# Performance work log

Hardware: AMD Instinct MI355X
Metric: run time of the kernel (lower is better)

Reference implementation:

```python
import jax, jax.numpy as jnp
import numpy as np
import math

B, S, D = 1, 2048, 2048
H, HD, KV = 16, 128, 1
E, F, TOPK = 8, 4096, 2
EPS = 1e-5


def setup_inputs() -> dict:
    key = jax.random.key(0)
    ks = jax.random.split(key, 14)
    sc = 0.02
    inp = {
        "x": jax.random.normal(ks[0], (B, S, D), dtype=jnp.float32),
        "wq": jax.random.normal(ks[1], (D, H * HD), dtype=jnp.float32) * sc,
        "wk": jax.random.normal(ks[2], (D, KV * HD), dtype=jnp.float32) * sc,
        "wv": jax.random.normal(ks[3], (D, KV * HD), dtype=jnp.float32) * sc,
        "wo": jax.random.normal(ks[4], (H * HD, D), dtype=jnp.float32) * sc,
        "w_router": jax.random.normal(ks[5], (D, E), dtype=jnp.float32) * sc,
        "w1": jax.random.normal(ks[6], (E, D, F), dtype=jnp.float32) * sc,
        "w3": jax.random.normal(ks[7], (E, D, F), dtype=jnp.float32) * sc,
        "w2": jax.random.normal(ks[8], (E, F, D), dtype=jnp.float32) * sc,
        "s_pre_mqa": jnp.ones((D,), dtype=jnp.float32),
        "s_post_mqa": jnp.ones((D,), dtype=jnp.float32),
        "s_pre_moe": jnp.ones((D,), dtype=jnp.float32),
        "s_post_moe": jnp.ones((D,), dtype=jnp.float32),
    }
    return inp


def _rmsnorm(x, scale):
    ms = jnp.mean(x * x, axis=-1, keepdims=True)
    return x * jax.lax.rsqrt(ms + EPS) * scale


def _mqa(h, wq, wk, wv, wo):
    b, s, _ = h.shape
    q = (h @ wq).reshape(b, s, H, HD)
    k = (h @ wk).reshape(b, s, KV, HD)
    v = (h @ wv).reshape(b, s, KV, HD)
    # repeat_interleave kv heads up to H (MQA)
    k = jnp.repeat(k, H // KV, axis=2)
    v = jnp.repeat(v, H // KV, axis=2)
    scale = 1.0 / math.sqrt(HD)
    scores = jnp.einsum("bqhd,bkhd->bhqk", q, k) * scale  # [B,H,S,S]
    causal = jnp.tril(jnp.ones((s, s), dtype=bool))
    scores = jnp.where(causal, scores, jnp.float32(-jnp.inf))
    attn = jax.nn.softmax(scores, axis=-1)
    out = jnp.einsum("bhqk,bkhd->bqhd", attn, v).reshape(b, s, H * HD)
    return out @ wo


def _moe(h, w_router, w1, w2, w3):
    logits = h @ w_router                        # [B,S,E]
    probs = jax.nn.softmax(logits, axis=-1)
    topv, topi = jax.lax.top_k(probs, TOPK)      # [B,S,K]
    topv = topv / jnp.sum(topv, axis=-1, keepdims=True)
    # combine weights per expert: [B,S,E]
    combine = jnp.sum(jax.nn.one_hot(topi, E, dtype=h.dtype) * topv[..., None], axis=-2)
    out = jnp.zeros_like(h)
    for e in range(E):  # fixed small expert count
        ye = (jax.nn.silu(h @ w1[e]) * (h @ w3[e])) @ w2[e]
        out = out + combine[..., e:e + 1] * ye
    return out, combine


def reference(x, wq, wk, wv, wo, w_router, w1, w2, w3,
              s_pre_mqa, s_post_mqa, s_pre_moe, s_post_moe):
    mqa_out = _mqa(_rmsnorm(x, s_pre_mqa), wq, wk, wv, wo)
    x = x + _rmsnorm(mqa_out, s_post_mqa)  # dropout p=0 (eval)
    moe_out, router_mask = _moe(_rmsnorm(x, s_pre_moe), w_router, w1, w2, w3)
    x = x + _rmsnorm(moe_out, s_post_moe)
    return x, router_mask
```

## Files before the change

### kernel.cpp

```cpp
#include <hip/hip_runtime.h>

#define S_LEN 2048
#define DM 2048
#define NHEAD 16
#define HDIM 128
#define NEXP 8
#define FF 4096
#define EPSV 1e-5f

typedef unsigned short u16;
typedef short bf16x8 __attribute__((ext_vector_type(8)));
typedef float f32x4 __attribute__((ext_vector_type(4)));

__device__ __forceinline__ f32x4 mfma16(bf16x8 a, bf16x8 b, f32x4 c) {
  return __builtin_amdgcn_mfma_f32_16x16x32_bf16(a, b, c, 0, 0, 0);
}

__device__ __forceinline__ float bf2f(u16 u) {
  union { unsigned int i; float f; } v; v.i = ((unsigned int)u) << 16; return v.f;
}
__device__ __forceinline__ u16 f2bf(float f) {
  union { float f; unsigned int i; } v; v.f = f;
  unsigned int u = v.i;
  return (u16)((u + 0x7fffu + ((u >> 16) & 1u)) >> 16);
}

__device__ __forceinline__ void gload_lds16(const u16* g, u16* l) {
  __builtin_amdgcn_global_load_lds(
      (const __attribute__((address_space(1))) unsigned int*)(unsigned long long)g,
      (__attribute__((address_space(3))) unsigned int*)(unsigned long long)l, 16, 0, 0);
}

__device__ __forceinline__ float blocksum(float v, float* sh) {
#pragma unroll
  for (int off = 32; off; off >>= 1) v += __shfl_xor(v, off, 64);
  const int w = threadIdx.x >> 6;
  if ((threadIdx.x & 63) == 0) sh[w] = v;
  __syncthreads();
  v = sh[0] + sh[1] + sh[2] + sh[3];
  __syncthreads();
  return v;
}

__global__ __launch_bounds__(256) void convsplit_kernel(
    const float* __restrict__ src, int ld, u16* __restrict__ dhi, u16* __restrict__ dlo) {
  __shared__ float tile[64][65];
  const int n0 = blockIdx.x * 64, k0 = blockIdx.y * 64;
  const int t = threadIdx.x;
  {
    int r = t >> 4, c4 = (t & 15) * 4;
#pragma unroll
    for (int i = 0; i < 4; ++i) {
      float4 v = *reinterpret_cast<const float4*>(src + (size_t)(k0 + r + i * 16) * ld + n0 + c4);
      tile[r + i * 16][c4 + 0] = v.x;
      tile[r + i * 16][c4 + 1] = v.y;
      tile[r + i * 16][c4 + 2] = v.z;
      tile[r + i * 16][c4 + 3] = v.w;
    }
  }
  __syncthreads();
#pragma unroll
  for (int i = 0; i < 2; ++i) {
    int idx = i * 256 + t;
    int n = idx >> 3, kc = (idx & 7) * 8;
    bf16x8 hi, lo;
#pragma unroll
    for (int j = 0; j < 8; ++j) {
      float f = tile[kc + j][n];
      u16 hv = f2bf(f);
      hi[j] = (short)hv;
      lo[j] = (short)f2bf(f - bf2f(hv));
    }
    size_t o = (size_t)(n0 + n) * 2048 + k0 + kc;
    *reinterpret_cast<bf16x8*>(dhi + o) = hi;
    *reinterpret_cast<bf16x8*>(dlo + o) = lo;
  }
}

__device__ __forceinline__ void convT_body(char* lds, const float* __restrict__ src,
                                           int R, int C, u16* __restrict__ dst,
                                           int nblk, int rblk, int e) {
  float(*tile)[65] = reinterpret_cast<float(*)[65]>(lds);
  const int n0 = nblk * 64, r0 = rblk * 64;
  const size_t bofs = (size_t)e * R * C;
  const int t = threadIdx.x;
  {
    int r = t >> 4, c4 = (t & 15) * 4;
#pragma unroll
    for (int i = 0; i < 4; ++i) {
      float4 v = *reinterpret_cast<const float4*>(src + bofs + (size_t)(r0 + r + i * 16) * C + n0 + c4);
      tile[r + i * 16][c4 + 0] = v.x;
      tile[r + i * 16][c4 + 1] = v.y;
      tile[r + i * 16][c4 + 2] = v.z;
      tile[r + i * 16][c4 + 3] = v.w;
    }
  }
  __syncthreads();
#pragma unroll
  for (int i = 0; i < 2; ++i) {
    int idx = i * 256 + t;
    int n = idx >> 3, kc = (idx & 7) * 8;
    bf16x8 pk;
#pragma unroll
    for (int j = 0; j < 8; ++j) pk[j] = (short)f2bf(tile[kc + j][n]);
    *reinterpret_cast<bf16x8*>(dst + bofs + (size_t)(n0 + n) * R + r0 + kc) = pk;
  }
}

__global__ __launch_bounds__(256) void rms_pre_kernel(
    const float* __restrict__ x, const float* __restrict__ s, u16* __restrict__ h1) {
  __shared__ float sh[4];
  const int row = blockIdx.x, t = threadIdx.x;
  const float* xr = x + (size_t)row * DM + t * 8;
  float4 a = *reinterpret_cast<const float4*>(xr);
  float4 b = *reinterpret_cast<const float4*>(xr + 4);
  float v[8] = {a.x, a.y, a.z, a.w, b.x, b.y, b.z, b.w};
  float ss = 0.f;
#pragma unroll
  for (int j = 0; j < 8; ++j) ss += v[j] * v[j];
  float inv = rsqrtf(blocksum(ss, sh) * (1.f / DM) + EPSV);
  const float* sp = s + t * 8;
  bf16x8 hi, lo;
#pragma unroll
  for (int j = 0; j < 8; ++j) {
    float val = v[j] * inv * sp[j];
    u16 hv = f2bf(val);
    hi[j] = (short)hv;
    lo[j] = (short)f2bf(val - bf2f(hv));
  }
  *reinterpret_cast<bf16x8*>(h1 + (size_t)row * 4096 + t * 8) = hi;
  *reinterpret_cast<bf16x8*>(h1 + (size_t)row * 4096 + 2048 + t * 8) = lo;
}

__device__ __forceinline__ void gemm3_body(
    char* lds, const u16* __restrict__ A, const u16* __restrict__ Bthi,
    const u16* __restrict__ Btlo, void* __restrict__ out,
    int mblk, int nblk, int mode, int ldc, int lo_off) {
  const int m0 = mblk * 128, n0 = nblk * 64;
  const int t = threadIdx.x, lane = t & 63, w = t >> 6;
  const int wm = (w >> 1) * 64, wn = (w & 1) * 32;
  const int l15 = lane & 15, lg = lane >> 4;
  const int wbase = t & ~63;

  u16* Ah = (u16*)lds;
  u16* Al = (u16*)(lds + 16384);
  u16* Bh = (u16*)(lds + 32768);
  u16* Bl = (u16*)(lds + 40960);

  const u16* Abh = A + (size_t)m0 * 4096;
  const u16* Abl = Abh + 2048;
  const u16* Bbh = Bthi + (size_t)n0 * 2048;
  const u16* Bbl = Btlo + (size_t)n0 * 2048;

  f32x4 acc[4][2];
#pragma unroll
  for (int m = 0; m < 4; ++m)
#pragma unroll
    for (int n = 0; n < 2; ++n) acc[m][n] = (f32x4){0.f, 0.f, 0.f, 0.f};

  for (int k0 = 0; k0 < 2048; k0 += 64) {
    __syncthreads();
#pragma unroll
    for (int i = 0; i < 4; ++i) {
      int p = i * 256 + t;
      int row = p >> 3;
      int csrc = (p & 7) ^ (row & 7);
      gload_lds16(Abh + (size_t)row * 4096 + k0 + csrc * 8, Ah + (i * 256 + wbase) * 8);
      gload_lds16(Abl + (size_t)row * 4096 + k0 + csrc * 8, Al + (i * 256 + wbase) * 8);
    }
#pragma unroll
    for (int i = 0; i < 2; ++i) {
      int p = i * 256 + t;
      int row = p >> 3;
      int csrc = (p & 7) ^ (row & 7);
      gload_lds16(Bbh + (size_t)row * 2048 + k0 + csrc * 8, Bh + (i * 256 + wbase) * 8);
      gload_lds16(Bbl + (size_t)row * 2048 + k0 + csrc * 8, Bl + (i * 256 + wbase) * 8);
    }
    __syncthreads();
#pragma unroll
    for (int kk = 0; kk < 2; ++kk) {
      bf16x8 ah[4], al[4], bh[2], bl[2];
#pragma unroll
      for (int m = 0; m < 4; ++m) {
        int row = wm + m * 16 + l15;
        int byte = row * 128 + (((kk * 4 + lg) * 16) ^ ((row & 7) << 4));
        ah[m] = *reinterpret_cast<const bf16x8*>((const char*)Ah + byte);
        al[m] = *reinterpret_cast<const bf16x8*>((const char*)Al + byte);
      }
#pragma unroll
      for (int n = 0; n < 2; ++n) {
        int row = wn + n * 16 + l15;
        int byte = row * 128 + (((kk * 4 + lg) * 16) ^ ((row & 7) << 4));
        bh[n] = *reinterpret_cast<const bf16x8*>((const char*)Bh + byte);
        bl[n] = *reinterpret_cast<const bf16x8*>((const char*)Bl + byte);
      }
#pragma unroll
      for (int m = 0; m < 4; ++m)
#pragma unroll
        for (int n = 0; n < 2; ++n) {
          acc[m][n] = mfma16(ah[m], bh[n], acc[m][n]);
          acc[m][n] = mfma16(al[m], bh[n], acc[m][n]);
          acc[m][n] = mfma16(ah[m], bl[n], acc[m][n]);
        }
    }
  }
#pragma unroll
  for (int m = 0; m < 4; ++m)
#pragma unroll
    for (int n = 0; n < 2; ++n)
#pragma unroll
      for (int r = 0; r < 4; ++r) {
        int row = m0 + wm + m * 16 + lg * 4 + r;
        int col = n0 + wn + n * 16 + l15;
        float v = acc[m][n][r];
        if (mode == 1) {
          u16* C = (u16*)out;
          u16 hv = f2bf(v);
          C[(size_t)row * ldc + col] = hv;
          C[(size_t)row * ldc + lo_off + col] = f2bf(v - bf2f(hv));
        } else {
          ((float*)out)[(size_t)row * ldc + col] = v;
        }
      }
}

__global__ __launch_bounds__(256) void gemm3_kernel(
    const u16* __restrict__ A, const u16* __restrict__ Bthi, const u16* __restrict__ Btlo,
    float* __restrict__ out) {
  __shared__ alignas(16) char lds[49152];
  gemm3_body(lds, A, Bthi, Btlo, out, blockIdx.x, blockIdx.y, 2, 2048, 0);
}

__global__ __launch_bounds__(256) void fat_qkv_conv(
    const u16* __restrict__ A, const u16* __restrict__ Bthi, const u16* __restrict__ Btlo,
    u16* __restrict__ QKV, const float* __restrict__ w1, const float* __restrict__ w3,
    u16* __restrict__ w1t, u16* __restrict__ w3t) {
  __shared__ alignas(16) char lds[49152];
  int bid = blockIdx.x;
  if (bid < 576) {
    gemm3_body(lds, A, Bthi, Btlo, QKV, bid % 16, bid / 16, 1, 4608, 2304);
  } else {
    int cid = bid - 576;
    if (cid < 16384)
      convT_body(lds, w1, 2048, 4096, w1t, cid % 64, (cid / 64) % 32, cid / 2048);
    else {
      cid -= 16384;
      convT_body(lds, w3, 2048, 4096, w3t, cid % 64, (cid / 64) % 32, cid / 2048);
    }
  }
}

__global__ __launch_bounds__(256) void vtrans_kernel(const u16* __restrict__ QKV,
                                                     u16* __restrict__ vt) {
  __shared__ u16 tile[64][65];
  const int s0 = blockIdx.x * 64, c0 = blockIdx.y * 64;
  const int t = threadIdx.x;
#pragma unroll
  for (int i = 0; i < 16; ++i) {
    int idx = i * 256 + t;
    int r = idx >> 6, c = idx & 63;
    int col = c0 + c;
    int src = (col < 128) ? (2176 + col) : (4480 + col - 128);
    tile[r][c] = QKV[(size_t)(s0 + r) * 4608 + src];
  }
  __syncthreads();
#pragma unroll
  for (int i = 0; i < 16; ++i) {
    int idx = i * 256 + t;
    int cc = idx >> 6, ss = idx & 63;
    vt[(size_t)(c0 + cc) * S_LEN + s0 + ss] = tile[ss][cc];
  }
}

__device__ __forceinline__ void attn_body(char* lds, const u16* __restrict__ QKV,
                                          const u16* __restrict__ vt, u16* __restrict__ Os,
                                          int bx, int h) {
  const int qb = 31 - bx;
  const int t = threadIdx.x, w = t >> 6, lane = t & 63;
  const int l15 = lane & 15, lg = lane >> 4;
  const int qr0 = qb * 64 + w * 16;
  const int qrow = qr0 + l15;

  u16* Ks = (u16*)lds;
  u16* Vs = (u16*)(lds + 17408);
  u16* myP = (u16*)(lds + 37888) + w * (16 * 72);

  bf16x8 qf[2][4];
#pragma unroll
  for (int p = 0; p < 2; ++p)
#pragma unroll
    for (int c = 0; c < 4; ++c)
      qf[p][c] = *reinterpret_cast<const bf16x8*>(QKV + (size_t)qrow * 4608 + p * 2304 +
                                                  h * 128 + c * 32 + lg * 8);

  f32x4 o[8];
#pragma unroll
  for (int n = 0; n < 8; ++n) o[n] = (f32x4){0.f, 0.f, 0.f, 0.f};
  f32x4 lracc = (f32x4){0.f, 0.f, 0.f, 0.f};
  bf16x8 onesf;
#pragma unroll
  for (int j = 0; j < 8; ++j) onesf[j] = (short)0x3F80;

  const float scale = 0.08838834764831845f;
  const int kend = qb * 64 + 64;

  for (int j0 = 0; j0 < kend; j0 += 32) {
    __syncthreads();
#pragma unroll
    for (int i = 0; i < 4; ++i) {
      int idx = i * 256 + t;
      int row = idx >> 5, seg = idx & 31;
      int srccol = (seg < 16) ? (2048 + seg * 8) : (4352 + (seg - 16) * 8);
      bf16x8 v = *reinterpret_cast<const bf16x8*>(QKV + (size_t)(j0 + row) * 4608 + srccol);
      *reinterpret_cast<bf16x8*>(&Ks[row * 272 + seg * 8]) = v;
    }
#pragma unroll
    for (int i = 0; i < 4; ++i) {
      int idx = i * 256 + t;
      int row = idx >> 2, seg = idx & 3;
      bf16x8 v = *reinterpret_cast<const bf16x8*>(vt + (size_t)row * S_LEN + j0 + seg * 8);
      *reinterpret_cast<bf16x8*>(&Vs[row * 40 + seg * 8]) = v;
    }
    __syncthreads();

    if (j0 > qr0 + 15) continue;
    f32x4 sc[2];
#pragma unroll
    for (int half = 0; half < 2; ++half) {
      const int kb = (half * 16 + l15) * 272;
      f32x4 a0 = (f32x4){0.f, 0.f, 0.f, 0.f};
      f32x4 a1 = (f32x4){0.f, 0.f, 0.f, 0.f};
      f32x4 a2 = (f32x4){0.f, 0.f, 0.f, 0.f};
#pragma unroll
      for (int cc = 0; cc < 4; ++cc) {
        bf16x8 kh = *reinterpret_cast<const bf16x8*>(&Ks[kb + cc * 32 + lg * 8]);
        a0 = mfma16(qf[0][cc], kh, a0);
        a1 = mfma16(qf[1][cc], kh, a1);
      }
#pragma unroll
      for (int cc = 0; cc < 4; ++cc) {
        bf16x8 kl = *reinterpret_cast<const bf16x8*>(&Ks[kb + 128 + cc * 32 + lg * 8]);
        a2 = mfma16(qf[0][cc], kl, a2);
      }
      f32x4 a = (a0 + a1) + a2;
#pragma unroll
      for (int r = 0; r < 4; ++r) {
        int rowg = qr0 + lg * 4 + r;
        int colg = j0 + half * 16 + l15;
        sc[half][r] = (colg <= rowg) ? a[r] * scale : -1e30f;
      }
    }
#pragma unroll
    for (int r = 0; r < 4; ++r) {
      float p0 = __expf(sc[0][r]);
      float p1 = __expf(sc[1][r]);
      int lrow = lg * 4 + r;
      u16 h0 = f2bf(p0), h1v = f2bf(p1);
      myP[lrow * 72 + l15] = h0;
      myP[lrow * 72 + 16 + l15] = h1v;
      myP[lrow * 72 + 32 + l15] = f2bf(p0 - bf2f(h0));
      myP[lrow * 72 + 48 + l15] = f2bf(p1 - bf2f(h1v));
    }
    bf16x8 pfh = *reinterpret_cast<const bf16x8*>(myP + l15 * 72 + lg * 8);
    bf16x8 pfl = *reinterpret_cast<const bf16x8*>(myP + l15 * 72 + 32 + lg * 8);

    lracc = mfma16(pfh, onesf, lracc);
    lracc = mfma16(pfl, onesf, lracc);

#pragma unroll
    for (int n = 0; n < 8; ++n) {
      bf16x8 vh = *reinterpret_cast<const bf16x8*>(&Vs[(n * 16 + l15) * 40 + lg * 8]);
      bf16x8 vl = *reinterpret_cast<const bf16x8*>(&Vs[(n * 16 + l15 + 128) * 40 + lg * 8]);
      o[n] = mfma16(pfh, vh, o[n]);
      o[n] = mfma16(pfl, vh, o[n]);
      o[n] = mfma16(pfh, vl, o[n]);
    }
  }
#pragma unroll
  for (int n = 0; n < 8; ++n)
#pragma unroll
    for (int r = 0; r < 4; ++r) {
      int rowg = qr0 + lg * 4 + r;
      float v = o[n][r] / lracc[r];
      u16 hv = f2bf(v);
      Os[(size_t)rowg * 4096 + h * 128 + n * 16 + l15] = hv;
      Os[(size_t)rowg * 4096 + 2048 + h * 128 + n * 16 + l15] = f2bf(v - bf2f(hv));
    }
}

__global__ __launch_bounds__(256) void fat_attn_conv(
    const u16* __restrict__ QKV, const u16* __restrict__ vt, u16* __restrict__ Os,
    const float* __restrict__ w2, u16* __restrict__ w2t) {
  __shared__ alignas(16) char lds[47104];
  int bid = blockIdx.x;
  if (bid < 512) {
    attn_body(lds, QKV, vt, Os, bid & 31, bid >> 5);
  } else {
    int cid = bid - 512;
    convT_body(lds, w2, 4096, 2048, w2t, cid % 32, (cid / 32) % 64, cid / 2048);
  }
}

__global__ __launch_bounds__(256) void rms_mid_router(
    const float* __restrict__ x, const float* __restrict__ mqa,
    const float* __restrict__ spost, const float* __restrict__ spre,
    const float* __restrict__ wr, float* __restrict__ x1, u16* __restrict__ h2b,
    float* __restrict__ comb, int* __restrict__ topi, float* __restrict__ topw,
    int* __restrict__ cnt) {
  __shared__ float sh1[4];
  __shared__ float sh2[4];
  __shared__ float red[4][8];
  __shared__ float lgits[8];
  const int row = blockIdx.x, t = threadIdx.x;
  const size_t base = (size_t)row * DM + t * 8;
  float mv[8];
  {
    float4 a0 = *reinterpret_cast<const float4*>(mqa + base);
    float4 b0 = *reinterpret_cast<const float4*>(mqa + base + 4);
    mv[0] = a0.x; mv[1] = a0.y; mv[2] = a0.z; mv[3] = a0.w;
    mv[4] = b0.x; mv[5] = b0.y; mv[6] = b0.z; mv[7] = b0.w;
  }
  float ss1 = 0.f;
#pragma unroll
  for (int j = 0; j < 8; ++j) ss1 += mv[j] * mv[j];
  float inv1 = rsqrtf(blocksum(ss1, sh1) * (1.f / DM) + EPSV);
  float4 xa = *reinterpret_cast<const float4*>(x + base);
  float4 xb = *reinterpret_cast<const float4*>(x + base + 4);
  float xv[8] = {xa.x, xa.y, xa.z, xa.w, xb.x, xb.y, xb.z, xb.w};
  float x1v[8];
  float ss2 = 0.f;
#pragma unroll
  for (int j = 0; j < 8; ++j) {
    x1v[j] = xv[j] + mv[j] * inv1 * spost[t * 8 + j];
    ss2 += x1v[j] * x1v[j];
  }
  float inv2 = rsqrtf(blocksum(ss2, sh2) * (1.f / DM) + EPSV);
  *reinterpret_cast<float4*>(x1 + base) = make_float4(x1v[0], x1v[1], x1v[2], x1v[3]);
  *reinterpret_cast<float4*>(x1 + base + 4) = make_float4(x1v[4], x1v[5], x1v[6], x1v[7]);
  float hv[8];
  bf16x8 hb;
#pragma unroll
  for (int j = 0; j < 8; ++j) {
    hv[j] = x1v[j] * inv2 * spre[t * 8 + j];
    hb[j] = (short)f2bf(hv[j]);
  }
  *reinterpret_cast<bf16x8*>(h2b + base) = hb;

  float acc[8] = {0.f, 0.f, 0.f, 0.f, 0.f, 0.f, 0.f, 0.f};
  const float* wrow = wr + (size_t)t * 64;
#pragma unroll
  for (int j = 0; j < 8; ++j) {
    const float* wj = wrow + j * 8;
#pragma unroll
    for (int e = 0; e < 8; ++e) acc[e] += hv[j] * wj[e];
  }
#pragma unroll
  for (int off = 32; off; off >>= 1)
#pragma unroll
    for (int e = 0; e < 8; ++e) acc[e] += __shfl_xor(acc[e], off, 64);
  const int w = t >> 6;
  if ((t & 63) == 0) {
#pragma unroll
    for (int e = 0; e < 8; ++e) red[w][e] = acc[e];
  }
  __syncthreads();
  if (t < 8) lgits[t] = red[0][t] + red[1][t] + red[2][t] + red[3][t];
  __syncthreads();
  if (t == 0) {
    float L[8], mx = -1e30f;
#pragma unroll
    for (int e = 0; e < 8; ++e) {
      L[e] = lgits[e];
      mx = fmaxf(mx, L[e]);
    }
    float p[8], s = 0.f;
#pragma unroll
    for (int e = 0; e < 8; ++e) {
      p[e] = expf(L[e] - mx);
      s += p[e];
    }
#pragma unroll
    for (int e = 0; e < 8; ++e) p[e] /= s;
    int e0 = 0;
    for (int e = 1; e < 8; ++e)
      if (p[e] > p[e0]) e0 = e;
    int e1 = (e0 == 0) ? 1 : 0;
    for (int e = 0; e < 8; ++e)
      if (e != e0 && p[e] > p[e1]) e1 = e;
    float ssum = p[e0] + p[e1];
    float w0 = p[e0] / ssum, w1 = p[e1] / ssum;
    for (int e = 0; e < 8; ++e)
      comb[(size_t)row * 8 + e] = (e == e0) ? w0 : ((e == e1) ? w1 : 0.f);
    topi[2 * row] = e0;
    topi[2 * row + 1] = e1;
    topw[2 * row] = w0;
    topw[2 * row + 1] = w1;
    atomicAdd(&cnt[e0], 1);
    atomicAdd(&cnt[e1], 1);
  }
}

__global__ void zero_meta_kernel(int* __restrict__ cnt) {
  if (threadIdx.x < NEXP) cnt[threadIdx.x] = 0;
}

__global__ void build_meta_kernel(const int* __restrict__ cnt, int* __restrict__ cursor,
                                  int* __restrict__ meta) {
  if (threadIdx.x != 0) return;
  int off = 0, nt = 0;
  for (int e = 0; e < NEXP; ++e) {
    int c = cnt[e];
    cursor[e] = off;
    int ntl = (c + 255) >> 8;
    for (int r = 0; r < ntl; ++r) {
      meta[8 + nt] = e;
      meta[64 + nt] = off + r * 256;
      int rem = c - r * 256;
      meta[120 + nt] = rem < 256 ? rem : 256;
      ++nt;
    }
    off += c;
  }
  meta[0] = nt;
}

__global__ void scatter_kernel(const int* __restrict__ topi, int* __restrict__ cursor,
                               int* __restrict__ ptok, int* __restrict__ pos_of) {
  int token = blockIdx.x * 256 + threadIdx.x;
  if (token >= S_LEN) return;
  for (int k = 0; k < 2; ++k) {
    int e = topi[2 * token + k];
    int pos = atomicAdd(&cursor[e], 1);
    ptok[pos] = token;
    pos_of[2 * token + k] = pos;
  }
}

__global__ __launch_bounds__(512) void moe_gemm1b(
    const u16* __restrict__ H2, const u16* __restrict__ W1t, const u16* __restrict__ W3t,
    u16* __restrict__ U, const int* __restrict__ meta, const int* __restrict__ ptok) {
  const int tile = blockIdx.x;
  if (tile >= meta[0]) return;
  const int e = meta[8 + tile], row0 = meta[64 + tile], rows = meta[120 + tile];
  const int n0 = blockIdx.y * 64;
  const u16* B1 = W1t + (size_t)e * FF * DM + (size_t)n0 * 2048;
  const u16* B3 = W3t + (size_t)e * FF * DM + (size_t)n0 * 2048;
  const int t = threadIdx.x, lane = t & 63, w = t >> 6;
  const int wm = (w >> 1) * 64, wn = (w & 1) * 32;
  const int l15 = lane & 15, lg = lane >> 4;
  const int wbase = t & ~63;

  __shared__ alignas(16) u16 As[16384];
  __shared__ alignas(16) u16 B1s[4096];
  __shared__ alignas(16) u16 B3s[4096];
  __shared__ int toks[256];
  if (t < 256) toks[t] = (t < rows) ? ptok[row0 + t] : ptok[row0];
  __syncthreads();

  f32x4 aG[4][2], aT[4][2];
#pragma unroll
  for (int m = 0; m < 4; ++m)
#pragma unroll
    for (int n = 0; n < 2; ++n) {
      aG[m][n] = (f32x4){0.f, 0.f, 0.f, 0.f};
      aT[m][n] = (f32x4){0.f, 0.f, 0.f, 0.f};
    }

  for (int k0 = 0; k0 < DM; k0 += 64) {
    __syncthreads();
#pragma unroll
    for (int i = 0; i < 4; ++i) {
      int p = i * 512 + t;
      int row = p >> 3;
      int csrc = (p & 7) ^ (row & 7);
      gload_lds16(H2 + (size_t)toks[row] * DM + k0 + csrc * 8, As + (i * 512 + wbase) * 8);
    }
    {
      int row = t >> 3;
      int csrc = (t & 7) ^ (row & 7);
      gload_lds16(B1 + (size_t)row * 2048 + k0 + csrc * 8, B1s + wbase * 8);
      gload_lds16(B3 + (size_t)row * 2048 + k0 + csrc * 8, B3s + wbase * 8);
    }
    __syncthreads();
#pragma unroll
    for (int kk = 0; kk < 2; ++kk) {
      bf16x8 af[4], b1f[2], b3f[2];
#pragma unroll
      for (int m = 0; m < 4; ++m) {
        int row = wm + m * 16 + l15;
        int byte = row * 128 + (((kk * 4 + lg) * 16) ^ ((row & 7) << 4));
        af[m] = *reinterpret_cast<const bf16x8*>((const char*)As + byte);
      }
#pragma unroll
      for (int n = 0; n < 2; ++n) {
        int row = wn + n * 16 + l15;
        int byte = row * 128 + (((kk * 4 + lg) * 16) ^ ((row & 7) << 4));
        b1f[n] = *reinterpret_cast<const bf16x8*>((const char*)B1s + byte);
        b3f[n] = *reinterpret_cast<const bf16x8*>((const char*)B3s + byte);
      }
#pragma unroll
      for (int m = 0; m < 4; ++m)
#pragma unroll
        for (int n = 0; n < 2; ++n) {
          aG[m][n] = mfma16(af[m], b1f[n], aG[m][n]);
          aT[m][n] = mfma16(af[m], b3f[n], aT[m][n]);
        }
    }
  }
#pragma unroll
  for (int m = 0; m < 4; ++m)
#pragma unroll
    for (int n = 0; n < 2; ++n)
#pragma unroll
      for (int r = 0; r < 4; ++r) {
        int lrow = wm + m * 16 + lg * 4 + r;
        if (lrow < rows) {
          float g = aG[m][n][r], tt = aT[m][n][r];
          float u = (g / (1.f + __expf(-g))) * tt;
          U[(size_t)(row0 + lrow) * FF + n0 + wn + n * 16 + l15] = f2bf(u);
        }
      }
}

__global__ __launch_bounds__(512) void moe_gemm2b(
    const u16* __restrict__ U, const u16* __restrict__ W2t, u16* __restrict__ Y,
    const int* __restrict__ meta) {
  const int tile = blockIdx.x;
  if (tile >= meta[0]) return;
  const int e = meta[8 + tile], row0 = meta[64 + tile], rows = meta[120 + tile];
  const int n0 = blockIdx.y * 128;
  const u16* Bb = W2t + (size_t)e * DM * FF + (size_t)n0 * 4096;
  const int t = threadIdx.x, lane = t & 63, w = t >> 6;
  const int wm = (w >> 1) * 64, wn = (w & 1) * 64;
  const int l15 = lane & 15, lg = lane >> 4;
  const int wbase = t & ~63;

  __shared__ alignas(16) u16 As[16384];
  __shared__ alignas(16) u16 Bs[8192];

  f32x4 acc[4][4];
#pragma unroll
  for (int m = 0; m < 4; ++m)
#pragma unroll
    for (int n = 0; n < 4; ++n) acc[m][n] = (f32x4){0.f, 0.f, 0.f, 0.f};

  for (int k0 = 0; k0 < FF; k0 += 64) {
    __syncthreads();
#pragma unroll
    for (int i = 0; i < 4; ++i) {
      int p = i * 512 + t;
      int row = p >> 3;
      int csrc = (p & 7) ^ (row & 7);
      gload_lds16(U + (size_t)(row0 + row) * FF + k0 + csrc * 8, As + (i * 512 + wbase) * 8);
    }
#pragma unroll
    for (int i = 0; i < 2; ++i) {
      int p = i * 512 + t;
      int row = p >> 3;
      int csrc = (p & 7) ^ (row & 7);
      gload_lds16(Bb + (size_t)row * 4096 + k0 + csrc * 8, Bs + (i * 512 + wbase) * 8);
    }
    __syncthreads();
#pragma unroll
    for (int kk = 0; kk < 2; ++kk) {
      bf16x8 af[4], bfr[4];
#pragma unroll
      for (int m = 0; m < 4; ++m) {
        int row = wm + m * 16 + l15;
        int byte = row * 128 + (((kk * 4 + lg) * 16) ^ ((row & 7) << 4));
        af[m] = *reinterpret_cast<const bf16x8*>((const char*)As + byte);
      }
#pragma unroll
      for (int n = 0; n < 4; ++n) {
        int row = wn + n * 16 + l15;
        int byte = row * 128 + (((kk * 4 + lg) * 16) ^ ((row & 7) << 4));
        bfr[n] = *reinterpret_cast<const bf16x8*>((const char*)Bs + byte);
      }
#pragma unroll
      for (int m = 0; m < 4; ++m)
#pragma unroll
        for (int n = 0; n < 4; ++n) acc[m][n] = mfma16(af[m], bfr[n], acc[m][n]);
    }
  }
#pragma unroll
  for (int m = 0; m < 4; ++m)
#pragma unroll
    for (int n = 0; n < 4; ++n)
#pragma unroll
      for (int r = 0; r < 4; ++r) {
        int lrow = wm + m * 16 + lg * 4 + r;
        if (lrow < rows)
          Y[(size_t)(row0 + lrow) * DM + n0 + wn + n * 16 + l15] = f2bf(acc[m][n][r]);
      }
}

__global__ __launch_bounds__(256) void moe_final_kernel(
    const float* __restrict__ x1, const u16* __restrict__ Y,
    const int* __restrict__ pos_of, const float* __restrict__ topw,
    const float* __restrict__ spost, float* __restrict__ xout) {
  __shared__ float sh[4];
  const int row = blockIdx.x, t = threadIdx.x;
  const int p0 = pos_of[2 * row], p1 = pos_of[2 * row + 1];
  const float w0 = topw[2 * row], w1 = topw[2 * row + 1];
  bf16x8 y0 = *reinterpret_cast<const bf16x8*>(Y + (size_t)p0 * DM + t * 8);
  bf16x8 y1 = *reinterpret_cast<const bf16x8*>(Y + (size_t)p1 * DM + t * 8);
  float mv[8];
  float ss = 0.f;
#pragma unroll
  for (int j = 0; j < 8; ++j) {
    mv[j] = w0 * bf2f((u16)y0[j]) + w1 * bf2f((u16)y1[j]);
    ss += mv[j] * mv[j];
  }
  float inv = rsqrtf(blocksum(ss, sh) * (1.f / DM) + EPSV);
  const size_t base = (size_t)row * DM + t * 8;
#pragma unroll
  for (int j = 0; j < 8; ++j)
    xout[base + j] = x1[base + j] + mv[j] * inv * spost[t * 8 + j];
}

extern "C" void kernel_launch(void* const* d_in, const int* in_sizes, int n_in,
                              void* d_out, int out_size, void* d_ws, size_t ws_size,
                              hipStream_t stream) {
  (void)in_sizes; (void)n_in; (void)out_size; (void)ws_size;
  const float* x = (const float*)d_in[0];
  const float* wq = (const float*)d_in[1];
  const float* wk = (const float*)d_in[2];
  const float* wv = (const float*)d_in[3];
  const float* wo = (const float*)d_in[4];
  const float* wrt = (const float*)d_in[5];
  const float* w1 = (const float*)d_in[6];
  const float* w3 = (const float*)d_in[7];
  const float* w2 = (const float*)d_in[8];
  const float* s_pre_mqa = (const float*)d_in[9];
  const float* s_post_mqa = (const float*)d_in[10];
  const float* s_pre_moe = (const float*)d_in[11];
  const float* s_post_moe = (const float*)d_in[12];

  float* xout = (float*)d_out;
  float* out_router = xout + (size_t)S_LEN * DM;

  char* wsp = (char*)d_ws;
  size_t off = 0;
  auto alloc = [&](size_t n) {
    char* p = wsp + off;
    off += (n + 255) & ~(size_t)255;
    return p;
  };
  u16* U = (u16*)alloc((size_t)4096 * FF * 2);
  u16* Y = (u16*)alloc((size_t)4096 * DM * 2);
  float* mqa = (float*)alloc((size_t)S_LEN * DM * 4);
  u16* h1s = (u16*)alloc((size_t)S_LEN * 4096 * 2);
  u16* attn_s = h1s;
  u16* Btq_hi = (u16*)alloc((size_t)2304 * 2048 * 2);
  u16* Btq_lo = (u16*)alloc((size_t)2304 * 2048 * 2);
  u16* Bto_hi = (u16*)alloc((size_t)2048 * 2048 * 2);
  u16* Bto_lo = (u16*)alloc((size_t)2048 * 2048 * 2);
  u16* QKV = (u16*)alloc((size_t)S_LEN * 4608 * 2);
  u16* vt = (u16*)alloc((size_t)256 * S_LEN * 2);
  float* x1 = (float*)alloc((size_t)S_LEN * DM * 4);
  u16* h2b = (u16*)alloc((size_t)S_LEN * DM * 2);
  int* topi = (int*)alloc(4096 * 4);
  float* topw = (float*)alloc(4096 * 4);
  int* pos_of = (int*)alloc(4096 * 4);
  int* ptok = (int*)alloc(4352 * 4);
  int* cnt = (int*)alloc(32 * 4);
  int* cursor = (int*)alloc(32 * 4);
  int* meta = (int*)alloc(256 * 4);
  u16* w1t = (u16*)alloc((size_t)NEXP * DM * FF * 2);
  u16* w3t = (u16*)alloc((size_t)NEXP * DM * FF * 2);
  u16* w2t = (u16*)alloc((size_t)NEXP * FF * DM * 2);

  dim3 B256(256);
  dim3 B512(512);

  convsplit_kernel<<<dim3(32, 32), B256, 0, stream>>>(wq, 2048, Btq_hi, Btq_lo);
  convsplit_kernel<<<dim3(2, 32), B256, 0, stream>>>(wk, 128, Btq_hi + (size_t)2048 * 2048,
                                                     Btq_lo + (size_t)2048 * 2048);
  convsplit_kernel<<<dim3(2, 32), B256, 0, stream>>>(wv, 128, Btq_hi + (size_t)2176 * 2048,
                                                     Btq_lo + (size_t)2176 * 2048);
  convsplit_kernel<<<dim3(32, 32), B256, 0, stream>>>(wo, 2048, Bto_hi, Bto_lo);

  rms_pre_kernel<<<dim3(S_LEN), B256, 0, stream>>>(x, s_pre_mqa, h1s);
  fat_qkv_conv<<<dim3(576 + 32768), B256, 0, stream>>>(h1s, Btq_hi, Btq_lo, QKV,
                                                       w1, w3, w1t, w3t);
  vtrans_kernel<<<dim3(32, 4), B256, 0, stream>>>(QKV, vt);
  fat_attn_conv<<<dim3(512 + 16384), B256, 0, stream>>>(QKV, vt, attn_s, w2, w2t);
  gemm3_kernel<<<dim3(16, 32), B256, 0, stream>>>(attn_s, Bto_hi, Bto_lo, mqa);
  zero_meta_kernel<<<dim3(1), dim3(64), 0, stream>>>(cnt);
  rms_mid_router<<<dim3(S_LEN), B256, 0, stream>>>(x, mqa, s_post_mqa, s_pre_moe, wrt,
                                                   x1, h2b, out_router, topi, topw, cnt);
  build_meta_kernel<<<dim3(1), dim3(64), 0, stream>>>(cnt, cursor, meta);
  scatter_kernel<<<dim3(8), B256, 0, stream>>>(topi, cursor, ptok, pos_of);
  moe_gemm1b<<<dim3(24, 64), B512, 0, stream>>>(h2b, w1t, w3t, U, meta, ptok);
  moe_gemm2b<<<dim3(24, 16), B512, 0, stream>>>(U, w2t, Y, meta);
  moe_final_kernel<<<dim3(S_LEN), B256, 0, stream>>>(x1, Y, pos_of, topw, s_post_moe, xout);
}
```

Before: 845.9 us.

## Rebalance weight conversions across fused kernels and fuse wo projection with w2 conversion

Redistributes the weight-conversion work so that each compute phase carries a conversion payload. The QKV GEMM now carries the w1 transpose and the wo split. Attention carries the w3 transpose. The wo GEMM becomes a fused kernel carrying the w2 transpose. The standalone wo convsplit launch is removed. The goal is to hide memory-bound conversion behind the compute-bound GEMM and attention blocks and to balance the load across the three fused launches, at the cost of more complex block dispatch and LDS sizing tied to the largest body.

Result: faster. 824.0 us (-2.6%).

```diff
diff --git a/kernel.cpp b/kernel.cpp
--- a/kernel.cpp
+++ b/kernel.cpp
@@ -42,10 +42,11 @@
   return v;
 }
 
-__global__ __launch_bounds__(256) void convsplit_kernel(
-    const float* __restrict__ src, int ld, u16* __restrict__ dhi, u16* __restrict__ dlo) {
-  __shared__ float tile[64][65];
-  const int n0 = blockIdx.x * 64, k0 = blockIdx.y * 64;
+__device__ __forceinline__ void convsplit_body(char* lds, const float* __restrict__ src,
+                                               int ld, u16* __restrict__ dhi,
+                                               u16* __restrict__ dlo, int nblk, int kblk) {
+  float(*tile)[65] = reinterpret_cast<float(*)[65]>(lds);
+  const int n0 = nblk * 64, k0 = kblk * 64;
   const int t = threadIdx.x;
   {
     int r = t >> 4, c4 = (t & 15) * 4;
@@ -75,6 +76,12 @@
     *reinterpret_cast<bf16x8*>(dhi + o) = hi;
     *reinterpret_cast<bf16x8*>(dlo + o) = lo;
   }
+}
+
+__global__ __launch_bounds__(256) void convsplit_kernel(
+    const float* __restrict__ src, int ld, u16* __restrict__ dhi, u16* __restrict__ dlo) {
+  __shared__ alignas(16) char lds[16640];
+  convsplit_body(lds, src, ld, dhi, dlo, blockIdx.x, blockIdx.y);
 }
 
 __device__ __forceinline__ void convT_body(char* lds, const float* __restrict__ src,
@@ -224,17 +231,10 @@
       }
 }
 
-__global__ __launch_bounds__(256) void gemm3_kernel(
-    const u16* __restrict__ A, const u16* __restrict__ Bthi, const u16* __restrict__ Btlo,
-    float* __restrict__ out) {
-  __shared__ alignas(16) char lds[49152];
-  gemm3_body(lds, A, Bthi, Btlo, out, blockIdx.x, blockIdx.y, 2, 2048, 0);
-}
-
 __global__ __launch_bounds__(256) void fat_qkv_conv(
     const u16* __restrict__ A, const u16* __restrict__ Bthi, const u16* __restrict__ Btlo,
-    u16* __restrict__ QKV, const float* __restrict__ w1, const float* __restrict__ w3,
-    u16* __restrict__ w1t, u16* __restrict__ w3t) {
+    u16* __restrict__ QKV, const float* __restrict__ w1, u16* __restrict__ w1t,
+    const float* __restrict__ wo, u16* __restrict__ BtoHi, u16* __restrict__ BtoLo) {
   __shared__ alignas(16) char lds[49152];
   int bid = blockIdx.x;
   if (bid < 576) {
@@ -245,7 +245,7 @@
       convT_body(lds, w1, 2048, 4096, w1t, cid % 64, (cid / 64) % 32, cid / 2048);
     else {
       cid -= 16384;
-      convT_body(lds, w3, 2048, 4096, w3t, cid % 64, (cid / 64) % 32, cid / 2048);
+      convsplit_body(lds, wo, 2048, BtoHi, BtoLo, cid & 31, cid >> 5);
     }
   }
 }
@@ -390,11 +390,24 @@
 
 __global__ __launch_bounds__(256) void fat_attn_conv(
     const u16* __restrict__ QKV, const u16* __restrict__ vt, u16* __restrict__ Os,
-    const float* __restrict__ w2, u16* __restrict__ w2t) {
+    const float* __restrict__ w3, u16* __restrict__ w3t) {
   __shared__ alignas(16) char lds[47104];
   int bid = blockIdx.x;
   if (bid < 512) {
     attn_body(lds, QKV, vt, Os, bid & 31, bid >> 5);
+  } else {
+    int cid = bid - 512;
+    convT_body(lds, w3, 2048, 4096, w3t, cid % 64, (cid / 64) % 32, cid / 2048);
+  }
+}
+
+__global__ __launch_bounds__(256) void fat_wo_conv(
+    const u16* __restrict__ A, const u16* __restrict__ Bthi, const u16* __restrict__ Btlo,
+    float* __restrict__ out, const float* __restrict__ w2, u16* __restrict__ w2t) {
+  __shared__ alignas(16) char lds[49152];
+  int bid = blockIdx.x;
+  if (bid < 512) {
+    gemm3_body(lds, A, Bthi, Btlo, out, bid & 15, bid >> 4, 2, 2048, 0);
   } else {
     int cid = bid - 512;
     convT_body(lds, w2, 4096, 2048, w2t, cid % 32, (cid / 32) % 64, cid / 2048);
@@ -778,14 +791,13 @@
                                                      Btq_lo + (size_t)2048 * 2048);
   convsplit_kernel<<<dim3(2, 32), B256, 0, stream>>>(wv, 128, Btq_hi + (size_t)2176 * 2048,
                                                      Btq_lo + (size_t)2176 * 2048);
-  convsplit_kernel<<<dim3(32, 32), B256, 0, stream>>>(wo, 2048, Bto_hi, Bto_lo);
 
   rms_pre_kernel<<<dim3(S_LEN), B256, 0, stream>>>(x, s_pre_mqa, h1s);
-  fat_qkv_conv<<<dim3(576 + 32768), B256, 0, stream>>>(h1s, Btq_hi, Btq_lo, QKV,
-                                                       w1, w3, w1t, w3t);
+  fat_qkv_conv<<<dim3(576 + 16384 + 1024), B256, 0, stream>>>(
+      h1s, Btq_hi, Btq_lo, QKV, w1, w1t, wo, Bto_hi, Bto_lo);
   vtrans_kernel<<<dim3(32, 4), B256, 0, stream>>>(QKV, vt);
-  fat_attn_conv<<<dim3(512 + 16384), B256, 0, stream>>>(QKV, vt, attn_s, w2, w2t);
-  gemm3_kernel<<<dim3(16, 32), B256, 0, stream>>>(attn_s, Bto_hi, Bto_lo, mqa);
+  fat_attn_conv<<<dim3(512 + 16384), B256, 0, stream>>>(QKV, vt, attn_s, w3, w3t);
+  fat_wo_conv<<<dim3(512 + 16384), B256, 0, stream>>>(attn_s, Bto_hi, Bto_lo, mqa, w2, w2t);
   zero_meta_kernel<<<dim3(1), dim3(64), 0, stream>>>(cnt);
   rms_mid_router<<<dim3(S_LEN), B256, 0, stream>>>(x, mqa, s_post_mqa, s_pre_moe, wrt,
                                                    x1, h2b, out_router, topi, topw, cnt);
```
